# Kernel tuning notes

Measured on AMD Instinct MI355X. Metric: run time of the kernel, lower is better.

The kernel has to match this reference:

```python
import jax, jax.numpy as jnp
import numpy as np

N_STEPS = 5
DT = 0.1
# radius fixed from initial sigma = 0.5 + 4.5*sigmoid(0.5) = 3.301 -> ceil(3*sigma) = 10
RADIUS = 10
SIZE = 2 * RADIUS + 1


def _pad1(x):
    return jnp.pad(x, ((0, 0), (0, 0), (1, 1), (1, 1)), mode='reflect')


def _spatial_gradient(x):
    p = _pad1(x)
    gy = (p[:, :, 2:, 1:-1] - p[:, :, :-2, 1:-1]) / 2.0
    gx = (p[:, :, 1:-1, 2:] - p[:, :, 1:-1, :-2]) / 2.0
    return gy, gx


def _laplacian(x):
    p = _pad1(x)
    return (p[:, :, :-2, 1:-1] + p[:, :, 2:, 1:-1]
            + p[:, :, 1:-1, :-2] + p[:, :, 1:-1, 2:] - 4.0 * x)


def _gaussian_blur(x, sigma):
    # differentiable kernel weights, fixed size (matches torch: radius from detached sigma)
    coords = jnp.arange(SIZE, dtype=x.dtype) - RADIUS
    k = jnp.exp(-coords ** 2 / (2.0 * sigma ** 2 + 1e-8))
    k = k / (k.sum() + 1e-8)
    xp = jnp.pad(x, ((0, 0), (0, 0), (0, 0), (RADIUS, RADIUS)), mode='reflect')
    out = jax.lax.conv_general_dilated(xp, k.reshape(1, 1, 1, SIZE), (1, 1), 'VALID')
    out = jnp.pad(out, ((0, 0), (0, 0), (RADIUS, RADIUS), (0, 0)), mode='reflect')
    out = jax.lax.conv_general_dilated(out, k.reshape(1, 1, SIZE, 1), (1, 1), 'VALID')
    return out


def _forward(image, lfd_map, alpha_raw, lambda_raw, log_sigma, log_beta, log_xi,
             eta_raw, nu_raw, log_gamma, omega_raw):
    sig = jax.nn.sigmoid
    alpha = 0.6 + 1.4 * sig(alpha_raw)
    lam = 0.01 + 0.19 * sig(lambda_raw)
    sigma = 0.5 + 4.5 * sig(log_sigma)
    beta = 1.0 + 4.0 * sig(log_beta)
    xi = 1.0 + 4.0 * sig(log_xi)
    eta = sig(eta_raw)
    nu = sig(nu_raw)
    gamma = 1.0 + 3.0 * sig(log_gamma)
    omega = sig(omega_raw)

    fractal_weight = jnp.clip(1.0 - omega * lfd_map, 0.0, 1.0)  # (B,1,H,W)
    u = image
    u0 = image
    for _ in range(N_STEPS):
        u_sigma = _gaussian_blur(u, sigma)
        gy, gx = _spatial_gradient(u)
        gys, gxs = _spatial_gradient(u_sigma)
        grad_mag = jnp.sqrt(gx ** 2 + gy ** 2 + 1e-8)
        grad_mag_s = jnp.sqrt(gxs ** 2 + gys ** 2 + 1e-8)
        lap_abs = jnp.abs(_laplacian(u))
        # conductance phi(s) = beta*sqrt(xi/(eta*s^2+eps)), clamped at 10
        phi = jnp.minimum(beta * jnp.sqrt(xi / (eta * grad_mag_s ** 2 + 1e-6)), 10.0)
        phi_f = phi * fractal_weight
        # curvature modulation psi'(s) = 1e-4*sqrt(nu*s^3+gamma), s = |grad u|*|lap u|
        s = grad_mag * lap_abs
        psi = 1e-4 * jnp.sqrt(nu * s ** 3 + gamma)
        pu = _pad1(u)
        dn = pu[:, :, :-2, 1:-1] - u
        dso = pu[:, :, 2:, 1:-1] - u
        de = pu[:, :, 1:-1, 2:] - u
        dw = pu[:, :, 1:-1, :-2] - u
        pp = _pad1(phi_f)
        div = (pp[:, :, :-2, 1:-1] * dn + pp[:, :, 2:, 1:-1] * dso
               + pp[:, :, 1:-1, 2:] * de + pp[:, :, 1:-1, :-2] * dw)
        du = alpha * psi * div - lam * (u - u0)
        u = jnp.clip(u + DT * du, 0.0, 1.0)
    edge_residual = jnp.abs(image - u)
    er_max = edge_residual.max(axis=(-2, -1), keepdims=True)
    edge_residual = edge_residual / (er_max + 1e-8)
    return u, edge_residual


def setup_inputs() -> dict:
    key = jax.random.key(0)
    k1, k2 = jax.random.split(key)
    B, H, W = 16, 512, 512
    image = jax.random.uniform(k1, (B, 1, H, W), jnp.float32)
    lfd_map = jax.random.uniform(k2, (B, 1, H, W), jnp.float32)
    f = lambda v: jnp.asarray(v, jnp.float32)
    return {
        'image': image, 'lfd_map': lfd_map,
        'alpha_raw': f(0.0), 'lambda_raw': f(-2.0), 'log_sigma': f(0.5),
        'log_beta': f(0.5), 'log_xi': f(0.5), 'eta_raw': f(0.3),
        'nu_raw': f(0.0), 'log_gamma': f(0.5), 'omega_raw': f(0.5),
    }


def reference(image, lfd_map, alpha_raw, lambda_raw, log_sigma, log_beta, log_xi,
              eta_raw, nu_raw, log_gamma, omega_raw):
    return _forward(image, lfd_map, alpha_raw, lambda_raw, log_sigma, log_beta,
                    log_xi, eta_raw, nu_raw, log_gamma, omega_raw)
```

## Files before the change

kernel.cpp:

```cpp
#include <hip/hip_runtime.h>
#include <math.h>

#define HH 512
#define WW 512
#define NPIX (16*HH*WW)
#define RAD 10
#define KS 21
#define TX 64
#define TY 32
#define TW 74
#define TH 42
#define TLW 76

__device__ __forceinline__ int refl(int v, int n){ v = v < 0 ? -v : v; return v >= n ? 2*n - 2 - v : v; }
__device__ __forceinline__ float sigm(float x){ return 1.f/(1.f+expf(-x)); }

__global__ void k_params(const float* a_raw, const float* l_raw, const float* lsig,
                         const float* lbeta, const float* lxi, const float* e_raw,
                         const float* n_raw, const float* lgam, const float* o_raw,
                         float* P)
{
    if (threadIdx.x || blockIdx.x) return;
    float sigma = 0.5f + 4.5f*sigm(lsig[0]);
    float beta  = 1.f + 4.f*sigm(lbeta[0]);
    float xi    = 1.f + 4.f*sigm(lxi[0]);
    float eta   = sigm(e_raw[0]);
    P[0] = 0.6f + 1.4f*sigm(a_raw[0]);
    P[1] = 0.01f + 0.19f*sigm(l_raw[0]);
    P[2] = beta;
    P[3] = xi;
    P[4] = eta;
    P[5] = sigm(n_raw[0]);
    P[6] = 1.f + 3.f*sigm(lgam[0]);
    P[7] = sigm(o_raw[0]);
    float kk[KS], s = 0.f;
    for (int i = 0; i < KS; ++i){ float c = (float)(i-RAD); kk[i] = expf(-c*c/(2.f*sigma*sigma+1e-8f)); s += kk[i]; }
    float inv = 1.f/(s+1e-8f);
    for (int i = 0; i < KS; ++i) P[8+i] = kk[i]*inv;
    P[30] = (beta*beta*xi >= 100.f*(eta*0.5000002f + 1e-6f)) ? 1.f : 0.f;
    for (int i = 0; i < 16; ++i) P[64+32*i] = 0.f;
}

__global__ __launch_bounds__(256, 4)
void k_mega(const float* __restrict__ img, const float* __restrict__ lfd,
            float* __restrict__ out_u, const float* __restrict__ P, float* Pmax)
{
    if (P[30] == 0.f) return;
    __shared__ float uA[TH][TLW];
    __shared__ float uB[TH][TLW];
    __shared__ float fwt[TH][TLW];
    __shared__ float red[4];
    const int tid = threadIdx.x;
    const int x0 = blockIdx.x*TX - 5, y0 = blockIdx.y*TY - 5;
    const int b = blockIdx.z;
    const float* ib = img + (b<<18);
    const float* lb = lfd + (b<<18);
    float* ob = out_u + (b<<18);
    const float a10 = 10.f*P[0], lam = P[1], nu = P[5], gam = P[6], omg = P[7];
    const bool bord = (blockIdx.x == 0) | (blockIdx.x == (WW/TX - 1)) |
                      (blockIdx.y == 0) | (blockIdx.y == (HH/TY - 1));

    for (int i = tid; i < TW*TH; i += 256){
        int r = i / TW, c = i - r*TW;
        int gx = x0 + c, gy = y0 + r;
        if (bord){ gx = refl(gx, WW); gy = refl(gy, HH); }
        int gi = gy*WW + gx;
        float u0 = ib[gi];
        uA[r][c] = u0;
        fwt[r][c] = fminf(fmaxf(1.f - omg*lb[gi], 0.f), 1.f);
    }
    __syncthreads();

    float mymax = 0.f;

#define DIFF_ITER(K, S, D, LAST) { \
    constexpr int w_ = TW - 2*(K), h_ = TH - 2*(K); \
    for (int i = tid; i < w_*h_; i += 256){ \
        int r = i / w_, c = i - r*w_; \
        int rr = r + (K), cc = c + (K); \
        float uc = S[rr][cc]; \
        float uN = S[rr-1][cc], uS = S[rr+1][cc]; \
        float uE = S[rr][cc+1], uW = S[rr][cc-1]; \
        float gyv = (uS-uN)*0.5f, gxv = (uE-uW)*0.5f; \
        float lap = uN+uS+uE+uW - 4.f*uc; \
        float gm = sqrtf(fmaf(gxv,gxv, fmaf(gyv,gyv, 1e-8f))); \
        float sv = gm*fabsf(lap); \
        float psi = 1e-4f*sqrtf(fmaf(nu, sv*sv*sv, gam)); \
        float dv = fwt[rr-1][cc]*(uN-uc) + fwt[rr+1][cc]*(uS-uc) \
                 + fwt[rr][cc+1]*(uE-uc) + fwt[rr][cc-1]*(uW-uc); \
        int gx = x0 + cc, gy = y0 + rr; \
        if (bord){ gx = refl(gx, WW); gy = refl(gy, HH); } \
        float u0v = ib[gy*WW + gx]; \
        float du = fmaf(a10*psi, dv, -lam*(uc - u0v)); \
        float un = fminf(fmaxf(fmaf(0.1f, du, uc), 0.f), 1.f); \
        if (LAST){ ob[gy*WW + gx] = un; mymax = fmaxf(mymax, fabsf(u0v - un)); } \
        else D[rr][cc] = un; \
    } \
    __syncthreads(); }

    DIFF_ITER(1, uA, uB, 0)
    DIFF_ITER(2, uB, uA, 0)
    DIFF_ITER(3, uA, uB, 0)
    DIFF_ITER(4, uB, uA, 0)
    DIFF_ITER(5, uA, uB, 1)
#undef DIFF_ITER

#pragma unroll
    for (int off = 32; off; off >>= 1) mymax = fmaxf(mymax, __shfl_down(mymax, off));
    if ((tid & 63) == 0) red[tid >> 6] = mymax;
    __syncthreads();
    if (tid == 0){
        float m = fmaxf(fmaxf(red[0],red[1]), fmaxf(red[2],red[3]));
        atomicMax((unsigned int*)(Pmax + 32*b), __float_as_uint(m));
    }
}

__global__ __launch_bounds__(256)
void k_iter(const float* __restrict__ src, const float* __restrict__ img,
            const float* __restrict__ lfd, float* __restrict__ dst,
            const float* __restrict__ P, float* Pmax, int do_max)
{
    if (P[30] != 0.f) return;
    __shared__ __attribute__((aligned(16))) float sh[56][72];
    __shared__ float su[36][72];
    __shared__ float ut[34][72];
    __shared__ float red[4];
    float (*pt)[72] = sh;

    const int tid = threadIdx.x;
    const int x0 = blockIdx.x * TX;
    const int y0 = blockIdx.y * TY;
    const int b  = blockIdx.z;
    const float* sb = src + (b << 18);
    const float* ib = img + (b << 18);
    const float* lb = lfd + (b << 18);
    float* db = dst + (b << 18);

    float kw[KS];
#pragma unroll
    for (int j = 0; j < KS; ++j) kw[j] = P[8 + j];
    const float alpha = P[0], lam = P[1], beta = P[2], xi = P[3];
    const float eta = P[4], nu = P[5], gam = P[6], omg = P[7];

#pragma unroll
    for (int p = 0; p < 9; ++p) {
        int i = tid + p * 256;
        if (i < 34 * 66) {
            int r = i / 66, c = i - r * 66;
            ut[r][c] = sb[refl(y0 - 1 + r, HH) * WW + refl(x0 - 1 + c, WW)];
        }
    }
#pragma unroll
    for (int p = 0; p < 4; ++p) {
        int i = tid + p * 256;
        if (i < 56 * 17) {
            int hr = i / 17, g = i - hr * 17;
            const float* row = sb + refl(y0 - 12 + hr, HH) * WW;
            int gxs = x0 - 12 + 4 * g;
            float w[24];
            if (gxs >= 0 && gxs + 23 < WW) {
                const float4* p4 = (const float4*)(row + gxs);
#pragma unroll
                for (int q = 0; q < 6; ++q) {
                    float4 v = p4[q];
                    w[4*q] = v.x; w[4*q+1] = v.y; w[4*q+2] = v.z; w[4*q+3] = v.w;
                }
            } else {
#pragma unroll
                for (int q = 0; q < 24; ++q) w[q] = row[refl(gxs + q, WW)];
            }
            float a0 = 0.f, a1 = 0.f, a2 = 0.f, a3 = 0.f;
#pragma unroll
            for (int j = 0; j < KS; ++j) {
                a0 = fmaf(kw[j], w[j],     a0);
                a1 = fmaf(kw[j], w[j + 1], a1);
                a2 = fmaf(kw[j], w[j + 2], a2);
                a3 = fmaf(kw[j], w[j + 3], a3);
            }
            float4 o; o.x = a0; o.y = a1; o.z = a2; o.w = a3;
            *(float4*)&sh[hr][4 * g] = o;
        }
    }
    __syncthreads();
#pragma unroll
    for (int p = 0; p < 3; ++p) {
        int i = tid + p * 256;
        if (i < 9 * 68) {
            int rg = i / 68, c = i - rg * 68;
            int r0 = rg * 4;
            float a0 = 0.f, a1 = 0.f, a2 = 0.f, a3 = 0.f;
#pragma unroll
            for (int q = 0; q < 24; ++q) {
                float s = sh[r0 + q][c];
                if (q <= 20)           a0 = fmaf(kw[q],     s, a0);
                if (q >= 1 && q <= 21) a1 = fmaf(kw[q - 1], s, a1);
                if (q >= 2 && q <= 22) a2 = fmaf(kw[q - 2], s, a2);
                if (q >= 3)            a3 = fmaf(kw[q - 3], s, a3);
            }
            su[r0][c] = a0; su[r0+1][c] = a1; su[r0+2][c] = a2; su[r0+3][c] = a3;
        }
    }
    __syncthreads();
#pragma unroll
    for (int p = 0; p < 9; ++p) {
        int i = tid + p * 256;
        if (i < 34 * 66) {
            int r = i / 66, c = i - r * 66;
            float gys = (su[r + 2][c + 1] - su[r][c + 1]) * 0.5f;
            float gxs = (su[r + 1][c + 2] - su[r + 1][c]) * 0.5f;
            float g2 = fmaf(gxs, gxs, fmaf(gys, gys, 1e-8f));
            float ph = fminf(beta * sqrtf(xi / fmaf(eta, g2, 1e-6f)), 10.f);
            float lv = lb[refl(y0 - 1 + r, HH) * WW + refl(x0 - 1 + c, WW)];
            float fw = fminf(fmaxf(1.f - omg * lv, 0.f), 1.f);
            pt[r][c] = ph * fw;
        }
    }
    __syncthreads();
    const int c = tid & 63, r0 = tid >> 6;
    float mymax = 0.f;
#pragma unroll
    for (int p = 0; p < 8; ++p) {
        int r = r0 + p * 4;
        float uc = ut[r + 1][c + 1];
        float uN = ut[r][c + 1],     uS = ut[r + 2][c + 1];
        float uE = ut[r + 1][c + 2], uW = ut[r + 1][c];
        float gy = (uS - uN) * 0.5f, gx = (uE - uW) * 0.5f;
        float lap = uN + uS + uE + uW - 4.f * uc;
        float gm = sqrtf(fmaf(gx, gx, fmaf(gy, gy, 1e-8f)));
        float s = gm * fabsf(lap);
        float psi = 1e-4f * sqrtf(fmaf(nu, s * s * s, gam));
        float pN = pt[r][c + 1],     pS = pt[r + 2][c + 1];
        float pE = pt[r + 1][c + 2], pW = pt[r + 1][c];
        float dv = pN * (uN - uc) + pS * (uS - uc) + pE * (uE - uc) + pW * (uW - uc);
        int gidx = (y0 + r) * WW + x0 + c;
        float u0v = ib[gidx];
        float du = alpha * psi * dv - lam * (uc - u0v);
        float un = fminf(fmaxf(fmaf(0.1f, du, uc), 0.f), 1.f);
        db[gidx] = un;
        mymax = fmaxf(mymax, fabsf(u0v - un));
    }
    if (do_max) {
#pragma unroll
        for (int off = 32; off; off >>= 1) mymax = fmaxf(mymax, __shfl_down(mymax, off));
        if ((tid & 63) == 0) red[tid >> 6] = mymax;
        __syncthreads();
        if (tid == 0) {
            float m = fmaxf(fmaxf(red[0], red[1]), fmaxf(red[2], red[3]));
            atomicMax((unsigned int*)(Pmax + 32 * b), __float_as_uint(m));
        }
    }
}

__global__ void k_res2(const float* __restrict__ img, const float* __restrict__ u,
                       float* __restrict__ r, const float* __restrict__ Pmax)
{
    int i = blockIdx.x * 256 + threadIdx.x;
    int b = i >> 16;
    float inv = 1.f / (Pmax[32 * b] + 1e-8f);
    float4 a = ((const float4*)img)[i];
    float4 c = ((const float4*)u)[i];
    float4 o;
    o.x = fabsf(a.x - c.x) * inv;
    o.y = fabsf(a.y - c.y) * inv;
    o.z = fabsf(a.z - c.z) * inv;
    o.w = fabsf(a.w - c.w) * inv;
    ((float4*)r)[i] = o;
}

extern "C" void kernel_launch(void* const* d_in, const int* in_sizes, int n_in,
                              void* d_out, int out_size, void* d_ws, size_t ws_size,
                              hipStream_t stream)
{
    const float* image = (const float*)d_in[0];
    const float* lfd   = (const float*)d_in[1];

    float* out_u = (float*)d_out;
    float* out_r = out_u + NPIX;

    float* uB = (float*)d_ws;
    float* P  = uB + NPIX;

    k_params<<<1, 64, 0, stream>>>((const float*)d_in[2], (const float*)d_in[3],
                                   (const float*)d_in[4], (const float*)d_in[5],
                                   (const float*)d_in[6], (const float*)d_in[7],
                                   (const float*)d_in[8], (const float*)d_in[9],
                                   (const float*)d_in[10], P);

    float* Pmax = P + 64;
    dim3 grd(WW/TX, HH/TY, 16), blk(256);

    k_mega<<<grd, blk, 0, stream>>>(image, lfd, out_u, P, Pmax);

    float* bufs[2] = { out_u, uB };
    for (int it = 0; it < 5; ++it) {
        const float* src = (it == 0) ? image : bufs[(it + 1) & 1];
        float* dstp = bufs[it & 1];
        k_iter<<<grd, blk, 0, stream>>>(src, image, lfd, dstp, P, Pmax, it == 4 ? 1 : 0);
    }

    k_res2<<<NPIX/1024, 256, 0, stream>>>(image, out_u, out_r, Pmax);
}
```

Before: 84.28 us.

## Rewrite fused 5-step diffusion kernel to keep the tile in registers with wave shuffles

The fused k_mega kernel, which runs when the conductance is saturated, now holds a 64x48 halo tile in per-thread registers (12 rows per wave, one column per lane) instead of double-buffered shared-memory tiles. East and west neighbours come from wave shuffles, and only the boundary rows between waves go through a small shared buffer. The grid changes to 54x38 output tiles with clamped origins. This removes the LDS traffic, the repeated global reads of u0, and the per-iteration index arithmetic, in exchange for more launched blocks, overlapping tiles where origins are clamped, and higher register pressure.

```diff
diff --git a/kernel.cpp b/kernel.cpp
--- a/kernel.cpp
+++ b/kernel.cpp
@@ -8,9 +8,8 @@
 #define KS 21
 #define TX 64
 #define TY 32
-#define TW 74
-#define TH 42
-#define TLW 76
+#define OTX 54
+#define OTY 38
 
 __device__ __forceinline__ int refl(int v, int n){ v = v < 0 ? -v : v; return v >= n ? 2*n - 2 - v : v; }
 __device__ __forceinline__ float sigm(float x){ return 1.f/(1.f+expf(-x)); }
@@ -46,71 +45,88 @@
             float* __restrict__ out_u, const float* __restrict__ P, float* Pmax)
 {
     if (P[30] == 0.f) return;
-    __shared__ float uA[TH][TLW];
-    __shared__ float uB[TH][TLW];
-    __shared__ float fwt[TH][TLW];
+    __shared__ float bnd[2][8][64];
     __shared__ float red[4];
-    const int tid = threadIdx.x;
-    const int x0 = blockIdx.x*TX - 5, y0 = blockIdx.y*TY - 5;
-    const int b = blockIdx.z;
+    const int tid  = threadIdx.x;
+    const int lane = tid & 63;
+    const int w    = tid >> 6;
+    const int ox = min((int)blockIdx.x * OTX, WW - OTX);
+    const int oy = min((int)blockIdx.y * OTY, HH - OTY);
+    const int b  = blockIdx.z;
     const float* ib = img + (b<<18);
     const float* lb = lfd + (b<<18);
     float* ob = out_u + (b<<18);
-    const float a10 = 10.f*P[0], lam = P[1], nu = P[5], gam = P[6], omg = P[7];
-    const bool bord = (blockIdx.x == 0) | (blockIdx.x == (WW/TX - 1)) |
-                      (blockIdx.y == 0) | (blockIdx.y == (HH/TY - 1));
-
-    for (int i = tid; i < TW*TH; i += 256){
-        int r = i / TW, c = i - r*TW;
-        int gx = x0 + c, gy = y0 + r;
-        if (bord){ gx = refl(gx, WW); gy = refl(gy, HH); }
-        int gi = gy*WW + gx;
-        float u0 = ib[gi];
-        uA[r][c] = u0;
-        fwt[r][c] = fminf(fmaxf(1.f - omg*lb[gi], 0.f), 1.f);
-    }
-    __syncthreads();
+    const float A = 1e-3f*P[0], lam = P[1], nu = P[5], gam = P[6], omg = P[7];
+
+    const int gxc = refl(ox - 5 + lane, WW);
+    const int t0  = 12*w;
+
+    float u[12], u0[12], fw[12];
+#pragma unroll
+    for (int j = 0; j < 12; ++j){
+        int gy = refl(oy - 5 + t0 + j, HH);
+        int gi = gy*WW + gxc;
+        float v = ib[gi];
+        u0[j] = v; u[j] = v;
+        fw[j] = fminf(fmaxf(1.f - omg*lb[gi], 0.f), 1.f);
+    }
+    float fwN0, fwS0;
+    { int gy = refl(oy - 6 + t0, HH);  fwN0 = fminf(fmaxf(1.f - omg*lb[gy*WW+gxc], 0.f), 1.f); }
+    { int gy = refl(oy + 7 + t0, HH);  fwS0 = fminf(fmaxf(1.f - omg*lb[gy*WW+gxc], 0.f), 1.f); }
+
+#pragma unroll
+    for (int K = 1; K <= 5; ++K){
+        const int p = K & 1;
+        bnd[p][2*w][lane]   = u[0];
+        bnd[p][2*w+1][lane] = u[11];
+        __syncthreads();
+        float uNb = (w > 0) ? bnd[p][2*w-1][lane] : 0.f;
+        float uSb = (w < 3) ? bnd[p][2*w+2][lane] : 0.f;
+        float um = uNb;
+#pragma unroll
+        for (int j = 0; j < 12; ++j){
+            const int t = t0 + j;
+            float cur = u[j];
+            float uS = (j == 11) ? uSb : u[j+1];
+            if (t >= K && t <= 47 - K){
+                float uN = um;
+                float uE = __shfl_down(cur, 1);
+                float uW = __shfl_up(cur, 1);
+                float fE = __shfl_down(fw[j], 1);
+                float fW = __shfl_up(fw[j], 1);
+                float fN = (j == 0)  ? fwN0 : fw[j-1];
+                float fS = (j == 11) ? fwS0 : fw[j+1];
+                float gyv = (uS - uN)*0.5f, gxv = (uE - uW)*0.5f;
+                float lap = (uN + uS) + (uE + uW) - 4.f*cur;
+                float g2 = fmaf(gxv, gxv, fmaf(gyv, gyv, 1e-8f));
+                float gm = sqrtf(g2);
+                float s  = gm*fabsf(lap);
+                float psi = sqrtf(fmaf(nu, s*s*s, gam));
+                float dv = fN*(uN-cur) + fS*(uS-cur) + fE*(uE-cur) + fW*(uW-cur);
+                float du = fmaf(A*psi, dv, -lam*(cur - u0[j]));
+                u[j] = fminf(fmaxf(fmaf(0.1f, du, cur), 0.f), 1.f);
+            }
+            um = cur;
+        }
+    }
 
     float mymax = 0.f;
-
-#define DIFF_ITER(K, S, D, LAST) { \
-    constexpr int w_ = TW - 2*(K), h_ = TH - 2*(K); \
-    for (int i = tid; i < w_*h_; i += 256){ \
-        int r = i / w_, c = i - r*w_; \
-        int rr = r + (K), cc = c + (K); \
-        float uc = S[rr][cc]; \
-        float uN = S[rr-1][cc], uS = S[rr+1][cc]; \
-        float uE = S[rr][cc+1], uW = S[rr][cc-1]; \
-        float gyv = (uS-uN)*0.5f, gxv = (uE-uW)*0.5f; \
-        float lap = uN+uS+uE+uW - 4.f*uc; \
-        float gm = sqrtf(fmaf(gxv,gxv, fmaf(gyv,gyv, 1e-8f))); \
-        float sv = gm*fabsf(lap); \
-        float psi = 1e-4f*sqrtf(fmaf(nu, sv*sv*sv, gam)); \
-        float dv = fwt[rr-1][cc]*(uN-uc) + fwt[rr+1][cc]*(uS-uc) \
-                 + fwt[rr][cc+1]*(uE-uc) + fwt[rr][cc-1]*(uW-uc); \
-        int gx = x0 + cc, gy = y0 + rr; \
-        if (bord){ gx = refl(gx, WW); gy = refl(gy, HH); } \
-        float u0v = ib[gy*WW + gx]; \
-        float du = fmaf(a10*psi, dv, -lam*(uc - u0v)); \
-        float un = fminf(fmaxf(fmaf(0.1f, du, uc), 0.f), 1.f); \
-        if (LAST){ ob[gy*WW + gx] = un; mymax = fmaxf(mymax, fabsf(u0v - un)); } \
-        else D[rr][cc] = un; \
-    } \
-    __syncthreads(); }
-
-    DIFF_ITER(1, uA, uB, 0)
-    DIFF_ITER(2, uB, uA, 0)
-    DIFF_ITER(3, uA, uB, 0)
-    DIFF_ITER(4, uB, uA, 0)
-    DIFF_ITER(5, uA, uB, 1)
-#undef DIFF_ITER
-
+    const bool colv = (lane >= 5) && (lane <= 58);
+#pragma unroll
+    for (int j = 0; j < 12; ++j){
+        const int t = t0 + j;
+        if (t >= 5 && t <= 42 && colv){
+            int gi = (oy + t - 5)*WW + (ox + lane - 5);
+            ob[gi] = u[j];
+            mymax = fmaxf(mymax, fabsf(u0[j] - u[j]));
+        }
+    }
 #pragma unroll
     for (int off = 32; off; off >>= 1) mymax = fmaxf(mymax, __shfl_down(mymax, off));
-    if ((tid & 63) == 0) red[tid >> 6] = mymax;
+    if (lane == 0) red[w] = mymax;
     __syncthreads();
     if (tid == 0){
-        float m = fmaxf(fmaxf(red[0],red[1]), fmaxf(red[2],red[3]));
+        float m = fmaxf(fmaxf(red[0], red[1]), fmaxf(red[2], red[3]));
         atomicMax((unsigned int*)(Pmax + 32*b), __float_as_uint(m));
     }
 }
@@ -157,25 +173,25 @@
             int hr = i / 17, g = i - hr * 17;
             const float* row = sb + refl(y0 - 12 + hr, HH) * WW;
             int gxs = x0 - 12 + 4 * g;
-            float w[24];
+            float wv[24];
             if (gxs >= 0 && gxs + 23 < WW) {
                 const float4* p4 = (const float4*)(row + gxs);
 #pragma unroll
                 for (int q = 0; q < 6; ++q) {
                     float4 v = p4[q];
-                    w[4*q] = v.x; w[4*q+1] = v.y; w[4*q+2] = v.z; w[4*q+3] = v.w;
+                    wv[4*q] = v.x; wv[4*q+1] = v.y; wv[4*q+2] = v.z; wv[4*q+3] = v.w;
                 }
             } else {
 #pragma unroll
-                for (int q = 0; q < 24; ++q) w[q] = row[refl(gxs + q, WW)];
+                for (int q = 0; q < 24; ++q) wv[q] = row[refl(gxs + q, WW)];
             }
             float a0 = 0.f, a1 = 0.f, a2 = 0.f, a3 = 0.f;
 #pragma unroll
             for (int j = 0; j < KS; ++j) {
-                a0 = fmaf(kw[j], w[j],     a0);
-                a1 = fmaf(kw[j], w[j + 1], a1);
-                a2 = fmaf(kw[j], w[j + 2], a2);
-                a3 = fmaf(kw[j], w[j + 3], a3);
+                a0 = fmaf(kw[j], wv[j],     a0);
+                a1 = fmaf(kw[j], wv[j + 1], a1);
+                a2 = fmaf(kw[j], wv[j + 2], a2);
+                a3 = fmaf(kw[j], wv[j + 3], a3);
             }
             float4 o; o.x = a0; o.y = a1; o.z = a2; o.w = a3;
             *(float4*)&sh[hr][4 * g] = o;
@@ -211,8 +227,8 @@
             float g2 = fmaf(gxs, gxs, fmaf(gys, gys, 1e-8f));
             float ph = fminf(beta * sqrtf(xi / fmaf(eta, g2, 1e-6f)), 10.f);
             float lv = lb[refl(y0 - 1 + r, HH) * WW + refl(x0 - 1 + c, WW)];
-            float fw = fminf(fmaxf(1.f - omg * lv, 0.f), 1.f);
-            pt[r][c] = ph * fw;
+            float fwv = fminf(fmaxf(1.f - omg * lv, 0.f), 1.f);
+            pt[r][c] = ph * fwv;
         }
     }
     __syncthreads();
@@ -287,10 +303,11 @@
                                    (const float*)d_in[10], P);
 
     float* Pmax = P + 64;
+
+    dim3 grd2((WW + OTX - 1)/OTX, (HH + OTY - 1)/OTY, 16);
+    k_mega<<<grd2, 256, 0, stream>>>(image, lfd, out_u, P, Pmax);
+
     dim3 grd(WW/TX, HH/TY, 16), blk(256);
-
-    k_mega<<<grd, blk, 0, stream>>>(image, lfd, out_u, P, Pmax);
-
     float* bufs[2] = { out_u, uB };
     for (int it = 0; it < 5; ++it) {
         const float* src = (it == 0) ? image : bufs[(it + 1) & 1];
```

Measured after the change: 95.95 us. +13.9%, slower.
